# Performance work log

Hardware: AMD Instinct MI355X
Metric: run time of the kernel (lower is better)

Reference implementation:

```python
import jax, jax.numpy as jnp
import numpy as np

B, I, J, NK = 2, 2048, 16, 2048
D_MODEL, D_HIDDEN, H = 256, 512, 8
D_K = D_HIDDEN // H


def setup_inputs() -> dict:
    key = jax.random.key(0)
    ks = jax.random.split(key, 12)
    s = 0.02
    return {
        "q": jax.random.normal(ks[0], (B, I, D_MODEL), jnp.float32),
        "k": jax.random.normal(ks[1], (B, NK, D_MODEL), jnp.float32),
        "pos": jax.random.normal(ks[2], (B, I, J, D_HIDDEN), jnp.float32),
        "local_idx": jax.random.randint(ks[3], (B, I, J), 0, NK, jnp.int64),
        "Wq": jax.random.normal(ks[4], (D_MODEL, D_HIDDEN), jnp.float32) * s,
        "Wkv": jax.random.normal(ks[5], (D_MODEL, 2 * D_HIDDEN), jnp.float32) * s,
        "W1": jax.random.normal(ks[6], (D_HIDDEN, D_HIDDEN), jnp.float32) * s,
        "b1": jnp.zeros((D_HIDDEN,), jnp.float32),
        "W2": jax.random.normal(ks[7], (D_HIDDEN, 2 * D_HIDDEN), jnp.float32) * s,
        "b2": jnp.zeros((2 * D_HIDDEN,), jnp.float32),
        "Wout": jax.random.normal(ks[8], (D_HIDDEN, D_MODEL), jnp.float32) * s,
    }


def reference(q, k, pos, local_idx, Wq, Wkv, W1, b1, W2, b2, Wout):
    b, i, j, _ = pos.shape
    scale = D_K ** (-0.5)
    # projections
    qh = (q @ Wq).reshape(b, i, H, D_K)                       # [b,i,h,d]
    kv = k @ Wkv                                               # [b,nk,2*dh]
    kk, vv = jnp.split(kv, 2, axis=-1)                         # each [b,nk,dh]
    # positional k/v bias MLP (Linear -> ReLU -> Linear)
    pos_kv = jax.nn.relu(pos @ W1 + b1) @ W2 + b2              # [b,i,j,2*dh]
    pos_k, pos_v = jnp.split(pos_kv.reshape(b, i, j, H, 2 * D_K), 2, axis=-1)
    # knn_gather: per-batch gather of neighbor features -> [b,i,j,dh]
    gather = jax.vmap(lambda x, idx: x[idx])
    kg = gather(kk, local_idx).reshape(b, i, j, H, D_K) + pos_k
    vg = gather(vv, local_idx).reshape(b, i, j, H, D_K) + pos_v
    # per-(i,j,h) attention over j neighbors
    attn = jnp.einsum('bihd,bijhd->bijh', qh, kg) * scale
    attn = jax.nn.softmax(attn, axis=2)
    agg = jnp.einsum('bijh,bijhd->bihd', attn, vg).reshape(b, i, H * D_K)
    # dropout is identity in eval mode
    return agg @ Wout
```

## Files before the change

kernel.cpp:

```cpp
#include <hip/hip_runtime.h>
#include <hip/hip_bf16.h>
#include <cstddef>


#define B_  2
#define I_  2048
#define J_  16
#define NK_ 2048
#define DM  256
#define DH  512
#define H_  8
#define DK  64
#define G_  4

typedef __attribute__((ext_vector_type(8))) __bf16 bf16x8;
typedef __attribute__((ext_vector_type(4))) float f32x4;
typedef __attribute__((ext_vector_type(8))) unsigned short ushort8;

__device__ inline unsigned short f2bf(float f) {
  unsigned int u = __builtin_bit_cast(unsigned int, f);
  u += 0x7FFFu + ((u >> 16) & 1u);
  return (unsigned short)(u >> 16);
}


template<int N>
__device__ void swz_body(const float* __restrict__ W,
                         unsigned short* __restrict__ Wf, int bid, int t)
{
  const int u  = bid * 256 + t;
  const int l  = u & 63;
  const int fi = u >> 6;
  const int ks = fi & 15;
  const int nt = fi >> 4;
  const int n  = nt * 16 + (l & 15);
  const int k0 = ks * 32 + (l >> 4) * 8;
  unsigned short tmp[8];
  #pragma unroll
  for (int j = 0; j < 8; ++j) tmp[j] = f2bf(W[(size_t)(k0 + j) * N + n]);
  *(ushort8*)&Wf[(size_t)u * 8] = *(const ushort8*)tmp;
}

template<int N, int CPT>
__device__ void proj_body(const float* __restrict__ X,
                          const float* __restrict__ W,
                          float* __restrict__ Y, float* Xs, int bid, int t)
{
  const int row0 = bid * 8;
  {
    const float4* x4 = (const float4*)(X + (size_t)row0 * DM);
    float4* s4 = (float4*)Xs;
    s4[t] = x4[t]; s4[t + 256] = x4[t + 256];
  }
  __syncthreads();

  float acc[8][CPT];
  #pragma unroll
  for (int r = 0; r < 8; ++r)
    #pragma unroll
    for (int u = 0; u < CPT; ++u) acc[r][u] = 0.f;

  const int c0 = t * CPT;
  for (int k = 0; k < DM; k += 4) {
    float4 xv[8];
    #pragma unroll
    for (int r = 0; r < 8; ++r) xv[r] = *(const float4*)&Xs[r * DM + k];
    float w4[4][CPT];
    #pragma unroll
    for (int kk = 0; kk < 4; ++kk) {
      if constexpr (CPT == 2) {
        const float2 wv = *(const float2*)&W[(size_t)(k + kk) * N + c0];
        w4[kk][0] = wv.x; w4[kk][1] = wv.y;
      } else {
        const float4 wv = *(const float4*)&W[(size_t)(k + kk) * N + c0];
        w4[kk][0] = wv.x; w4[kk][1] = wv.y; w4[kk][2] = wv.z; w4[kk][3] = wv.w;
      }
    }
    #pragma unroll
    for (int kk = 0; kk < 4; ++kk) {
      #pragma unroll
      for (int r = 0; r < 8; ++r) {
        const float xs = ((const float*)&xv[r])[kk];
        #pragma unroll
        for (int u = 0; u < CPT; ++u) acc[r][u] += xs * w4[kk][u];
      }
    }
  }
  #pragma unroll
  for (int r = 0; r < 8; ++r)
    #pragma unroll
    for (int u = 0; u < CPT; ++u)
      Y[(size_t)(row0 + r) * N + c0 + u] = acc[r][u];
}

__global__ __launch_bounds__(256) void pre_kernel(
    const float* __restrict__ q, const float* __restrict__ k,
    const float* __restrict__ Wq, const float* __restrict__ Wkv,
    const float* __restrict__ W1, const float* __restrict__ W2,
    float* __restrict__ qh_ws, float* __restrict__ kv_ws,
    unsigned short* __restrict__ W1f, unsigned short* __restrict__ W2f)
{
  __shared__ float Xs[8 * DM];
  const int bid = blockIdx.x;
  const int t = threadIdx.x;
  if (bid < 512)        proj_body<DH, 2>   (q, Wq,  qh_ws, Xs, bid, t);
  else if (bid < 1024)  proj_body<2*DH, 4> (k, Wkv, kv_ws, Xs, bid - 512, t);
  else if (bid < 1152)  swz_body<DH>       (W1, W1f, bid - 1024, t);
  else                  swz_body<2*DH>     (W2, W2f, bid - 1152, t);
}

__global__ __launch_bounds__(256, 2) void fused_mfma(
    const float* __restrict__ pos, const int* __restrict__ lidx,
    const float* __restrict__ qh, const float* __restrict__ kv,
    const unsigned short* __restrict__ W1f, const float* __restrict__ b1,
    const unsigned short* __restrict__ W2f, const float* __restrict__ b2,
    const float* __restrict__ Wout, float* __restrict__ out)
{
  __shared__ unsigned short s_a[G_ * 16 * 64 * 8];
  __shared__ float s_agg2[G_ * DH];

  const int t    = threadIdx.x;
  const int lane = t & 63;
  const int w    = t >> 6;
  const int g    = lane >> 4;
  const int c16  = lane & 15;
  const int bi0  = blockIdx.x * G_;
  const int b    = bi0 >> 11;

  bool idx64;
  {
    int orv = 0;
    #pragma unroll
    for (int m = 0; m < 16; ++m) orv |= lidx[2 * m + 1];
    idx64 = (orv == 0);
  }
  int idxr[G_][4];
  #pragma unroll
  for (int mt = 0; mt < G_; ++mt)
    #pragma unroll
    for (int r = 0; r < 4; ++r) {
      const int e = (bi0 + mt) * J_ + g * 4 + r;
      idxr[mt][r] = idx64 ? lidx[2 * e] : lidx[e];
    }

  #pragma unroll
  for (int it = 0; it < 16; ++it) {
    const int u  = t + it * 256;
    const int fi = u >> 6, ld = u & 63;
    const int mt = fi >> 4, ks = fi & 15;
    const int row = mt * 16 + (ld & 15);
    const int col = ks * 32 + (ld >> 4) * 8;
    const float* src = pos + (size_t)(bi0 * J_ + row) * DH + col;
    const float4 v0 = *(const float4*)src;
    const float4 v1 = *(const float4*)(src + 4);
    unsigned short tmp[8];
    tmp[0] = f2bf(v0.x); tmp[1] = f2bf(v0.y); tmp[2] = f2bf(v0.z); tmp[3] = f2bf(v0.w);
    tmp[4] = f2bf(v1.x); tmp[5] = f2bf(v1.y); tmp[6] = f2bf(v1.z); tmp[7] = f2bf(v1.w);
    *(ushort8*)&s_a[(size_t)u * 8] = *(const ushort8*)tmp;
  }
  __syncthreads();

  const f32x4 zero4 = {0.f, 0.f, 0.f, 0.f};

  f32x4 acc1[G_][8];
  #pragma unroll
  for (int mt = 0; mt < G_; ++mt)
    #pragma unroll
    for (int nt = 0; nt < 8; ++nt) acc1[mt][nt] = zero4;

  for (int ks = 0; ks < 16; ++ks) {
    bf16x8 a[G_];
    #pragma unroll
    for (int mt = 0; mt < G_; ++mt)
      a[mt] = *(const bf16x8*)&s_a[((mt * 16 + ks) * 64 + lane) * 8];
    bf16x8 bfr[8];
    #pragma unroll
    for (int nt = 0; nt < 8; ++nt)
      bfr[nt] = *(const bf16x8*)&W1f[((size_t)((w * 8 + nt) * 16 + ks) * 64 + lane) * 8];
    #pragma unroll
    for (int nt = 0; nt < 8; ++nt)
      #pragma unroll
      for (int mt = 0; mt < G_; ++mt)
        acc1[mt][nt] = __builtin_amdgcn_mfma_f32_16x16x32_bf16(a[mt], bfr[nt], acc1[mt][nt], 0, 0, 0);
  }
  __syncthreads();

  #pragma unroll
  for (int nt = 0; nt < 8; ++nt) {
    const int col  = (w * 8 + nt) * 16 + c16;
    const float bb = b1[col];
    const int ks2  = col >> 5;
    const int lsel = ((col >> 3) & 3) * 16;
    const int bj   = col & 7;
    #pragma unroll
    for (int mt = 0; mt < G_; ++mt)
      #pragma unroll
      for (int r = 0; r < 4; ++r) {
        const float hv = fmaxf(acc1[mt][nt][r] + bb, 0.f);
        s_a[((mt * 16 + ks2) * 64 + (g * 4 + r) + lsel) * 8 + bj] = f2bf(hv);
      }
  }
  __syncthreads();

  #pragma unroll
  for (int p = 0; p < 2; ++p) {
    const int h = 2 * w + p;
    f32x4 acc2[G_][8];
    #pragma unroll
    for (int mt = 0; mt < G_; ++mt)
      #pragma unroll
      for (int tt = 0; tt < 8; ++tt) acc2[mt][tt] = zero4;

    for (int ks = 0; ks < 16; ++ks) {
      bf16x8 a[G_];
      #pragma unroll
      for (int mt = 0; mt < G_; ++mt)
        a[mt] = *(const bf16x8*)&s_a[((mt * 16 + ks) * 64 + lane) * 8];
      bf16x8 bfr[8];
      #pragma unroll
      for (int tt = 0; tt < 8; ++tt)
        bfr[tt] = *(const bf16x8*)&W2f[((size_t)((h * 8 + tt) * 16 + ks) * 64 + lane) * 8];
      #pragma unroll
      for (int tt = 0; tt < 8; ++tt)
        #pragma unroll
        for (int mt = 0; mt < G_; ++mt)
          acc2[mt][tt] = __builtin_amdgcn_mfma_f32_16x16x32_bf16(a[mt], bfr[tt], acc2[mt][tt], 0, 0, 0);
    }

    float b2k[4], b2v[4], qv[G_][4];
    #pragma unroll
    for (int tt = 0; tt < 4; ++tt) {
      b2k[tt] = b2[h * 128 + tt * 16 + c16];
      b2v[tt] = b2[h * 128 + 64 + tt * 16 + c16];
    }
    #pragma unroll
    for (int mt = 0; mt < G_; ++mt)
      #pragma unroll
      for (int tt = 0; tt < 4; ++tt)
        qv[mt][tt] = qh[(size_t)(bi0 + mt) * DH + h * 64 + tt * 16 + c16];

    #pragma unroll
    for (int mt = 0; mt < G_; ++mt) {
      float pj[4];
      #pragma unroll
      for (int r = 0; r < 4; ++r) {
        const float* kvrow = kv + ((size_t)b * NK_ + idxr[mt][r]) * (2 * DH);
        float s = 0.f;
        #pragma unroll
        for (int tt = 0; tt < 4; ++tt) {
          const int d = h * 64 + tt * 16 + c16;
          const float kg = acc2[mt][tt][r] + b2k[tt] + kvrow[d];
          s += qv[mt][tt] * kg;
          acc2[mt][4 + tt][r] += b2v[tt] + kvrow[DH + d];
        }
        s += __shfl_xor(s, 1);  s += __shfl_xor(s, 2);
        s += __shfl_xor(s, 4);  s += __shfl_xor(s, 8);
        pj[r] = s * 0.125f;
      }
      float mx = fmaxf(fmaxf(pj[0], pj[1]), fmaxf(pj[2], pj[3]));
      mx = fmaxf(mx, __shfl_xor(mx, 16));
      mx = fmaxf(mx, __shfl_xor(mx, 32));
      float sum = 0.f;
      #pragma unroll
      for (int r = 0; r < 4; ++r) { pj[r] = __expf(pj[r] - mx); sum += pj[r]; }
      sum += __shfl_xor(sum, 16);
      sum += __shfl_xor(sum, 32);
      const float inv = 1.f / sum;
      #pragma unroll
      for (int r = 0; r < 4; ++r) pj[r] *= inv;
      #pragma unroll
      for (int tt = 0; tt < 4; ++tt) {
        float a_ = pj[0] * acc2[mt][4 + tt][0] + pj[1] * acc2[mt][4 + tt][1]
                 + pj[2] * acc2[mt][4 + tt][2] + pj[3] * acc2[mt][4 + tt][3];
        a_ += __shfl_xor(a_, 16);
        a_ += __shfl_xor(a_, 32);
        if (g == 0)
          s_agg2[mt * DH + h * 64 + tt * 16 + c16] = a_;
      }
    }
  }
  __syncthreads();

  float* s_part = (float*)s_a;
  f32x4 oacc[G_];
  #pragma unroll
  for (int i = 0; i < G_; ++i) oacc[i] = zero4;
  for (int c4 = 0; c4 < 32; ++c4) {
    const int c = w * 128 + c4 * 4;
    f32x4 ag[G_];
    #pragma unroll
    for (int i = 0; i < G_; ++i) ag[i] = *(const f32x4*)&s_agg2[i * DH + c];
    #pragma unroll
    for (int cc = 0; cc < 4; ++cc) {
      const f32x4 wv = *(const f32x4*)&Wout[(size_t)(c + cc) * DM + lane * 4];
      #pragma unroll
      for (int i = 0; i < G_; ++i) oacc[i] += wv * ag[i][cc];
    }
  }
  #pragma unroll
  for (int i = 0; i < G_; ++i)
    *(f32x4*)&s_part[(w * G_ + i) * DM + lane * 4] = oacc[i];
  __syncthreads();

  #pragma unroll
  for (int i = 0; i < G_; ++i) {
    const float o = s_part[(0 * G_ + i) * DM + t] + s_part[(1 * G_ + i) * DM + t]
                  + s_part[(2 * G_ + i) * DM + t] + s_part[(3 * G_ + i) * DM + t];
    out[(size_t)(bi0 + i) * DM + t] = o;
  }
}

extern "C" void kernel_launch(void* const* d_in, const int* in_sizes, int n_in,
                              void* d_out, int out_size, void* d_ws, size_t ws_size,
                              hipStream_t stream)
{
  const float* q    = (const float*)d_in[0];
  const float* k    = (const float*)d_in[1];
  const float* pos  = (const float*)d_in[2];
  const int*   lidx = (const int*)d_in[3];
  const float* Wq   = (const float*)d_in[4];
  const float* Wkv  = (const float*)d_in[5];
  const float* W1   = (const float*)d_in[6];
  const float* b1   = (const float*)d_in[7];
  const float* W2   = (const float*)d_in[8];
  const float* b2   = (const float*)d_in[9];
  const float* Wout = (const float*)d_in[10];
  float* out = (float*)d_out;

  float* qh_ws = (float*)d_ws;
  float* kv_ws = qh_ws + (size_t)(B_ * I_) * DH;
  unsigned short* W1f = (unsigned short*)(kv_ws + (size_t)(B_ * NK_) * (2 * DH));
  unsigned short* W2f = W1f + (size_t)DH * DH;

  pre_kernel<<<1408, 256, 0, stream>>>(q, k, Wq, Wkv, W1, W2,
                                       qh_ws, kv_ws, W1f, W2f);
  fused_mfma<<<(B_ * I_) / G_, 256, 0, stream>>>(pos, lidx, qh_ws, kv_ws,
                                                 W1f, b1, W2f, b2, Wout, out);
}
```

Measured before the change: 431.6 us.

## Replace scalar fp32 q/kv projections with bf16 MFMA kernel using pre-swizzled weights

The q and k projections now run on bf16 MFMA instructions instead of scalar FP32 FMAs. Wq and Wkv are first swizzled into the MFMA fragment layout by a separate weight-prep kernel, and a new 128-block kernel computes 64-row tiles. This targets compute cost in the pre-stage but adds a kernel launch and bf16 rounding of the projection inputs. The low block count may leave much of the GPU idle.

```diff
diff --git a/kernel.cpp b/kernel.cpp
--- a/kernel.cpp
+++ b/kernel.cpp
@@ -23,16 +23,22 @@
   return (unsigned short)(u >> 16);
 }
 
-
-template<int N>
+__device__ inline bf16x8 cvt8(float4 a, float4 b) {
+  bf16x8 r;
+  r[0] = (__bf16)a.x; r[1] = (__bf16)a.y; r[2] = (__bf16)a.z; r[3] = (__bf16)a.w;
+  r[4] = (__bf16)b.x; r[5] = (__bf16)b.y; r[6] = (__bf16)b.z; r[7] = (__bf16)b.w;
+  return r;
+}
+
+template<int N, int KS>
 __device__ void swz_body(const float* __restrict__ W,
                          unsigned short* __restrict__ Wf, int bid, int t)
 {
   const int u  = bid * 256 + t;
   const int l  = u & 63;
   const int fi = u >> 6;
-  const int ks = fi & 15;
-  const int nt = fi >> 4;
+  const int ks = fi % KS;
+  const int nt = fi / KS;
   const int n  = nt * 16 + (l & 15);
   const int k0 = ks * 32 + (l >> 4) * 8;
   unsigned short tmp[8];
@@ -41,72 +47,81 @@
   *(ushort8*)&Wf[(size_t)u * 8] = *(const ushort8*)tmp;
 }
 
-template<int N, int CPT>
-__device__ void proj_body(const float* __restrict__ X,
-                          const float* __restrict__ W,
-                          float* __restrict__ Y, float* Xs, int bid, int t)
-{
-  const int row0 = bid * 8;
-  {
-    const float4* x4 = (const float4*)(X + (size_t)row0 * DM);
-    float4* s4 = (float4*)Xs;
-    s4[t] = x4[t]; s4[t + 256] = x4[t + 256];
-  }
-  __syncthreads();
-
-  float acc[8][CPT];
-  #pragma unroll
-  for (int r = 0; r < 8; ++r)
-    #pragma unroll
-    for (int u = 0; u < CPT; ++u) acc[r][u] = 0.f;
-
-  const int c0 = t * CPT;
-  for (int k = 0; k < DM; k += 4) {
-    float4 xv[8];
-    #pragma unroll
-    for (int r = 0; r < 8; ++r) xv[r] = *(const float4*)&Xs[r * DM + k];
-    float w4[4][CPT];
-    #pragma unroll
-    for (int kk = 0; kk < 4; ++kk) {
-      if constexpr (CPT == 2) {
-        const float2 wv = *(const float2*)&W[(size_t)(k + kk) * N + c0];
-        w4[kk][0] = wv.x; w4[kk][1] = wv.y;
-      } else {
-        const float4 wv = *(const float4*)&W[(size_t)(k + kk) * N + c0];
-        w4[kk][0] = wv.x; w4[kk][1] = wv.y; w4[kk][2] = wv.z; w4[kk][3] = wv.w;
-      }
-    }
-    #pragma unroll
-    for (int kk = 0; kk < 4; ++kk) {
-      #pragma unroll
-      for (int r = 0; r < 8; ++r) {
-        const float xs = ((const float*)&xv[r])[kk];
-        #pragma unroll
-        for (int u = 0; u < CPT; ++u) acc[r][u] += xs * w4[kk][u];
-      }
-    }
-  }
-  #pragma unroll
-  for (int r = 0; r < 8; ++r)
-    #pragma unroll
-    for (int u = 0; u < CPT; ++u)
-      Y[(size_t)(row0 + r) * N + c0 + u] = acc[r][u];
-}
-
-__global__ __launch_bounds__(256) void pre_kernel(
-    const float* __restrict__ q, const float* __restrict__ k,
+__global__ __launch_bounds__(256) void swz_kernel(
     const float* __restrict__ Wq, const float* __restrict__ Wkv,
     const float* __restrict__ W1, const float* __restrict__ W2,
-    float* __restrict__ qh_ws, float* __restrict__ kv_ws,
+    unsigned short* __restrict__ Wqf, unsigned short* __restrict__ Wkvf,
     unsigned short* __restrict__ W1f, unsigned short* __restrict__ W2f)
 {
-  __shared__ float Xs[8 * DM];
   const int bid = blockIdx.x;
   const int t = threadIdx.x;
-  if (bid < 512)        proj_body<DH, 2>   (q, Wq,  qh_ws, Xs, bid, t);
-  else if (bid < 1024)  proj_body<2*DH, 4> (k, Wkv, kv_ws, Xs, bid - 512, t);
-  else if (bid < 1152)  swz_body<DH>       (W1, W1f, bid - 1024, t);
-  else                  swz_body<2*DH>     (W2, W2f, bid - 1152, t);
+  if (bid < 64)        swz_body<DH, 8>    (Wq,  Wqf,  bid,       t);
+  else if (bid < 192)  swz_body<2*DH, 8>  (Wkv, Wkvf, bid - 64,  t);
+  else if (bid < 320)  swz_body<DH, 16>   (W1,  W1f,  bid - 192, t);
+  else                 swz_body<2*DH, 16> (W2,  W2f,  bid - 320, t);
+}
+
+__global__ __launch_bounds__(256) void proj_mfma(
+    const float* __restrict__ q, const float* __restrict__ k,
+    const unsigned short* __restrict__ Wqf,
+    const unsigned short* __restrict__ Wkvf,
+    float* __restrict__ qh_ws, float* __restrict__ kv_ws)
+{
+  const int t    = threadIdx.x;
+  const int lane = t & 63;
+  const int w    = t >> 6;
+  const int g    = lane >> 4;
+  const int c16  = lane & 15;
+
+  const bool is_kv = blockIdx.x >= 64;
+  const int  bid   = is_kv ? (int)blockIdx.x - 64 : (int)blockIdx.x;
+  const int  row0  = bid * 64;
+  const float* X = is_kv ? k : q;
+  const unsigned short* Wf = is_kv ? Wkvf : Wqf;
+  const int  N     = is_kv ? 2 * DH : DH;
+  float*     Y     = is_kv ? kv_ws : qh_ws;
+  const int  passes = is_kv ? 2 : 1;
+
+  const f32x4 zero4 = {0.f, 0.f, 0.f, 0.f};
+  const float* pa = X + (size_t)(row0 + (lane & 15)) * DM + ((lane >> 4) << 3);
+
+  for (int hp = 0; hp < passes; ++hp) {
+    f32x4 acc[G_][8];
+    #pragma unroll
+    for (int mt = 0; mt < G_; ++mt)
+      #pragma unroll
+      for (int nt = 0; nt < 8; ++nt) acc[mt][nt] = zero4;
+
+    for (int ks = 0; ks < 8; ++ks) {
+      bf16x8 a[G_];
+      #pragma unroll
+      for (int mt = 0; mt < G_; ++mt) {
+        const float* s = pa + (size_t)mt * 16 * DM + ks * 32;
+        a[mt] = cvt8(*(const float4*)s, *(const float4*)(s + 4));
+      }
+      bf16x8 bfr[8];
+      #pragma unroll
+      for (int nt = 0; nt < 8; ++nt) {
+        const int ntg = hp * 32 + w * 8 + nt;
+        bfr[nt] = *(const bf16x8*)&Wf[((size_t)(ntg * 8 + ks) * 64 + lane) * 8];
+      }
+      #pragma unroll
+      for (int nt = 0; nt < 8; ++nt)
+        #pragma unroll
+        for (int mt = 0; mt < G_; ++mt)
+          acc[mt][nt] = __builtin_amdgcn_mfma_f32_16x16x32_bf16(a[mt], bfr[nt], acc[mt][nt], 0, 0, 0);
+    }
+
+    #pragma unroll
+    for (int nt = 0; nt < 8; ++nt) {
+      const int col = hp * 512 + (w * 8 + nt) * 16 + c16;
+      #pragma unroll
+      for (int mt = 0; mt < G_; ++mt)
+        #pragma unroll
+        for (int r = 0; r < 4; ++r)
+          Y[(size_t)(row0 + mt * 16 + g * 4 + r) * N + col] = acc[mt][nt][r];
+    }
+  }
 }
 
 __global__ __launch_bounds__(256, 2) void fused_mfma(
@@ -329,11 +344,13 @@
 
   float* qh_ws = (float*)d_ws;
   float* kv_ws = qh_ws + (size_t)(B_ * I_) * DH;
-  unsigned short* W1f = (unsigned short*)(kv_ws + (size_t)(B_ * NK_) * (2 * DH));
-  unsigned short* W2f = W1f + (size_t)DH * DH;
-
-  pre_kernel<<<1408, 256, 0, stream>>>(q, k, Wq, Wkv, W1, W2,
-                                       qh_ws, kv_ws, W1f, W2f);
+  unsigned short* W1f  = (unsigned short*)(kv_ws + (size_t)(B_ * NK_) * (2 * DH));
+  unsigned short* W2f  = W1f + (size_t)DH * DH;
+  unsigned short* Wqf  = W2f + (size_t)DH * (2 * DH);
+  unsigned short* Wkvf = Wqf + (size_t)DM * DH;
+
+  swz_kernel<<<576, 256, 0, stream>>>(Wq, Wkv, W1, W2, Wqf, Wkvf, W1f, W2f);
+  proj_mfma<<<128, 256, 0, stream>>>(q, k, Wqf, Wkvf, qh_ws, kv_ws);
   fused_mfma<<<(B_ * I_) / G_, 256, 0, stream>>>(pos, lidx, qh_ws, kv_ws,
                                                  W1f, b1, W2f, b2, Wout, out);
 }
```

Result: faster. 393.6 us (-8.8%).
